# Optimization experiments

Measured on AMD Instinct MI355X. Metric: run time of the kernel, lower is better.

The kernel has to match this reference:

```python
import jax, jax.numpy as jnp
import numpy as np

B, N, E = 32, 128, 8192        # graphs, nodes/graph, edges total
IN, ED, H = 64, 32, 128        # node feat, edge feat, hidden
K1, K2, K3 = 64, 32, 16        # ceil(0.5*N) cascade from TopKPooling(ratio=0.5)
EPS = 1e-5


def setup_inputs():
    key = jax.random.key(0)
    ks = jax.random.split(key, 20)
    def rn(i, shape, s=1.0):
        return jax.random.normal(ks[i], shape, dtype=jnp.float32) * s
    x = rn(0, (B * N, IN))
    edge_attr = rn(1, (E, ED))
    epg = E // B  # edges per graph (intra-graph only)
    src = jax.random.randint(ks[2], (B, epg), 0, N)
    dst = jax.random.randint(ks[3], (B, epg), 0, N)
    off = (jnp.arange(B) * N)[:, None]
    edge_index = jnp.stack([(src + off).reshape(-1), (dst + off).reshape(-1)]).astype(jnp.int32)
    batch = jnp.repeat(jnp.arange(B), N).astype(jnp.int32)
    p = {}
    p['nn1_w'] = rn(4, (ED, IN * H), 0.05); p['nn1_b'] = jnp.zeros((IN * H,), jnp.float32)
    p['root1'] = rn(5, (IN, H), 0.1);       p['bias1'] = jnp.zeros((H,), jnp.float32)
    p['nn2_w'] = rn(6, (ED, H * H), 0.05);  p['nn2_b'] = jnp.zeros((H * H,), jnp.float32)
    p['root2'] = rn(7, (H, H), 0.1);        p['bias2'] = jnp.zeros((H,), jnp.float32)
    p['nn3_w'] = rn(8, (ED, H * H), 0.05);  p['nn3_b'] = jnp.zeros((H * H,), jnp.float32)
    p['root3'] = rn(9, (H, H), 0.1);        p['bias3'] = jnp.zeros((H,), jnp.float32)
    for k in ('1', '2', '3'):
        p['gamma' + k] = jnp.ones((H,), jnp.float32)
        p['beta' + k] = jnp.zeros((H,), jnp.float32)
    p['pw1'] = rn(10, (H,), 0.1); p['pw2'] = rn(11, (H,), 0.1); p['pw3'] = rn(12, (H,), 0.1)
    p['lin1_w'] = rn(13, (H, H // 2), 0.1); p['lin1_b'] = jnp.zeros((H // 2,), jnp.float32)
    p['lin2_w'] = rn(14, (H // 2, 1), 0.1); p['lin2_b'] = jnp.zeros((1,), jnp.float32)
    return dict(x=x, edge_index=edge_index, edge_attr=edge_attr, batch=batch, **p)


def _nnconv(x, src, dst, emask, eattr, nn_w, nn_b, root, bias, cin, cout, n_nodes):
    # per-edge weight matrix from edge MLP: [E, cin, cout]
    w = (eattr @ nn_w + nn_b).reshape(-1, cin, cout)
    msg = jnp.einsum('ei,eio->eo', x[src], w) * emask[:, None]  # per-edge matvec
    agg = jnp.zeros((n_nodes, cout), x.dtype).at[dst].add(msg)  # scatter-add aggr
    return agg + x @ root + bias


def _bn(x, gamma, beta):
    mu = x.mean(0)
    var = x.var(0)
    return gamma * (x - mu) * jax.lax.rsqrt(var + EPS) + beta


def _topk_pool(x, src, dst, emask, pw, nb, npg, k):
    # PyG TopKPooling: score = tanh((x.p)/||p||); keep top ceil(ratio*n) per graph
    score = jnp.tanh((x @ pw) / jnp.linalg.norm(pw))            # [nb*npg]
    _, idx = jax.lax.top_k(score.reshape(nb, npg), k)           # [nb, k]
    perm = (idx + (jnp.arange(nb) * npg)[:, None]).reshape(-1)  # global node ids
    x_new = x[perm] * score[perm][:, None]
    mapping = jnp.full((nb * npg,), -1, jnp.int32).at[perm].set(
        jnp.arange(nb * k, dtype=jnp.int32))
    ns, nd = mapping[src], mapping[dst]
    valid = (ns >= 0) & (nd >= 0) & emask   # filter_adj via mask, static shapes
    return x_new, jnp.where(valid, ns, 0), jnp.where(valid, nd, 0), valid


def _forward(x, edge_attr, nn1_w, nn1_b, root1, bias1, gamma1, beta1, pw1,
             nn2_w, nn2_b, root2, bias2, gamma2, beta2, pw2,
             nn3_w, nn3_b, root3, bias3, gamma3, beta3, pw3,
             lin1_w, lin1_b, lin2_w, lin2_b, edge_index):
    src0, dst0 = edge_index[0], edge_index[1]
    m0 = jnp.ones((E,), bool)
    h = _nnconv(x, src0, dst0, m0, edge_attr, nn1_w, nn1_b, root1, bias1, IN, H, B * N)
    h = jax.nn.relu(_bn(h, gamma1, beta1))
    h, s1, d1, m1 = _topk_pool(h, src0, dst0, m0, pw1, B, N, K1)
    h = _nnconv(h, s1, d1, m1, edge_attr, nn2_w, nn2_b, root2, bias2, H, H, B * K1)
    h = jax.nn.relu(_bn(h, gamma2, beta2))
    h, s2, d2, m2 = _topk_pool(h, s1, d1, m1, pw2, B, K1, K2)
    h = _nnconv(h, s2, d2, m2, edge_attr, nn3_w, nn3_b, root3, bias3, H, H, B * K2)
    h = jax.nn.relu(_bn(h, gamma3, beta3))
    h, _, _, _ = _topk_pool(h, s2, d2, m2, pw3, B, K2, K3)
    g = h.reshape(B, K3, H).mean(axis=1)          # global_mean_pool (equal-size graphs)
    g = jax.nn.relu(g @ lin1_w + lin1_b)          # dropout is identity in eval mode
    return jax.nn.sigmoid(g @ lin2_w + lin2_b)    # [B, 1]


def reference(x, edge_index, edge_attr, batch,
              nn1_w, nn1_b, root1, bias1, nn2_w, nn2_b, root2, bias2,
              nn3_w, nn3_b, root3, bias3, gamma1, beta1, gamma2, beta2,
              gamma3, beta3, pw1, pw2, pw3, lin1_w, lin1_b, lin2_w, lin2_b):
    return _forward(x, edge_attr, nn1_w, nn1_b, root1, bias1, gamma1, beta1, pw1,
                    nn2_w, nn2_b, root2, bias2, gamma2, beta2, pw2,
                    nn3_w, nn3_b, root3, bias3, gamma3, beta3, pw3,
                    lin1_w, lin1_b, lin2_w, lin2_b, edge_index)
```

## Files before the change

kernel.cpp:

```cpp
#include <hip/hip_runtime.h>

#define E_TOT 8192
#define NB    32
#define H     128
#define EPG   256
#define NDT   34
#define YD    33
#define YCOLS (YD * H)

typedef __attribute__((ext_vector_type(8))) short bf16x8;
typedef __attribute__((ext_vector_type(4))) float f32x4;

__device__ __forceinline__ unsigned short bf16_rne(float f) {
    unsigned int u = __float_as_uint(f);
    unsigned int r = (u + 0x7FFFu + ((u >> 16) & 1u)) >> 16;
    return (unsigned short)r;
}
__device__ __forceinline__ float bf16_to_f32(unsigned short h) {
    return __uint_as_float(((unsigned int)h) << 16);
}

__device__ __forceinline__ void gload_lds16(const void* g, void* l) {
    __builtin_amdgcn_global_load_lds(
        (const __attribute__((address_space(1))) unsigned int*)g,
        (__attribute__((address_space(3))) unsigned int*)l, 16, 0, 0);
}

template<int CIN>
__global__ __launch_bounds__(128)
void build_A(const float* __restrict__ x, unsigned short* __restrict__ A)
{
    const int v = blockIdx.x;
    unsigned short* row = A + (size_t)v * (3 * CIN);
    for (int i = threadIdx.x; i < CIN; i += 128) {
        const float val = x[(size_t)v * CIN + i];
        const unsigned short h = bf16_rne(val);
        const unsigned short l = bf16_rne(val - bf16_to_f32(h));
        row[i] = h; row[CIN + i] = h; row[2 * CIN + i] = l;
    }
}

template<int CIN>
__global__ __launch_bounds__(256)
void build_Bt(const float* __restrict__ nnw, const float* __restrict__ nnb,
              const float* __restrict__ root, unsigned short* __restrict__ Bt)
{
    const int d  = blockIdx.x;
    const int i0 = blockIdx.y * 32;
    const float* __restrict__ W =
        (d < 32) ? (nnw + (size_t)d * CIN * 128) : ((d == 32) ? nnb : root);

    __shared__ unsigned short LHI[128][40];
    __shared__ unsigned short LLO[128][40];

    for (int idx = threadIdx.x; idx < 32 * 128; idx += 256) {
        const int ii = idx >> 7, o = idx & 127;
        const float val = W[(size_t)(i0 + ii) * 128 + o];
        const unsigned short h = bf16_rne(val);
        const unsigned short l = bf16_rne(val - bf16_to_f32(h));
        LHI[o][ii] = h; LLO[o][ii] = l;
    }
    __syncthreads();

    const int o    = threadIdx.x & 127;
    const int half = threadIdx.x >> 7;
    unsigned short* dst = Bt + (size_t)(d * 128 + o) * (3 * CIN);
    const uint4* hs = (const uint4*)&LHI[o][0];
    const uint4* ls = (const uint4*)&LLO[o][0];
    if (half == 0) {
        uint4* p = (uint4*)(dst + i0);
        p[0] = hs[0]; p[1] = hs[1]; p[2] = hs[2]; p[3] = hs[3];
        uint4* q = (uint4*)(dst + 2 * CIN + i0);
        q[0] = ls[0]; q[1] = ls[1]; q[2] = ls[2]; q[3] = ls[3];
    } else {
        uint4* p = (uint4*)(dst + CIN + i0);
        p[0] = hs[0]; p[1] = hs[1]; p[2] = hs[2]; p[3] = hs[3];
    }
}

template<int K3>
__global__ __launch_bounds__(256)
void ygemm_mfma(const unsigned short* __restrict__ A,
                const unsigned short* __restrict__ Bt,
                float* __restrict__ Y,
                const float* __restrict__ bias,
                float* __restrict__ h)
{
    __shared__ unsigned short Alds[128 * 32];
    __shared__ unsigned short Blds[128 * 32];

    const int lane = threadIdx.x & 63;
    const int w    = threadIdx.x >> 6;
    const int wm = w >> 1, wn = w & 1;
    const int v0 = blockIdx.x * 128;
    const int n0 = blockIdx.y * 128;

    f32x4 acc[4][4];
    #pragma unroll
    for (int i = 0; i < 4; ++i)
        #pragma unroll
        for (int j = 0; j < 4; ++j)
            acc[i][j] = (f32x4)(0.0f);

    const int arow = lane >> 2;
    const int acol = (lane & 3) * 8;
    const int koff = (lane >> 4) * 8;
    const int mrow = lane & 15;

    for (int k0 = 0; k0 < K3; k0 += 32) {
        __syncthreads();
        #pragma unroll
        for (int t = 0; t < 2; ++t) {
            const int c = w * 2 + t;
            const int r = c * 16 + arow;
            gload_lds16(A  + (size_t)(v0 + r) * K3 + k0 + acol, &Alds[c * 512]);
            gload_lds16(Bt + (size_t)(n0 + r) * K3 + k0 + acol, &Blds[c * 512]);
        }
        __syncthreads();

        bf16x8 a[4], b[4];
        #pragma unroll
        for (int f = 0; f < 4; ++f) {
            a[f] = *(const bf16x8*)&Alds[(wm * 64 + f * 16 + mrow) * 32 + koff];
            b[f] = *(const bf16x8*)&Blds[(wn * 64 + f * 16 + mrow) * 32 + koff];
        }
        #pragma unroll
        for (int fm = 0; fm < 4; ++fm)
            #pragma unroll
            for (int fn = 0; fn < 4; ++fn)
                acc[fm][fn] = __builtin_amdgcn_mfma_f32_16x16x32_bf16(
                    a[fm], b[fn], acc[fm][fn], 0, 0, 0);
    }

    const int crow = (lane >> 4) * 4;
    const int ccol = lane & 15;
    const bool is_root = (blockIdx.y == YD);
    #pragma unroll
    for (int fm = 0; fm < 4; ++fm) {
        const int gr = v0 + wm * 64 + fm * 16 + crow;
        #pragma unroll
        for (int fn = 0; fn < 4; ++fn) {
            const int col = wn * 64 + fn * 16 + ccol;
            if (is_root) {
                const float bv = bias[col];
                #pragma unroll
                for (int r = 0; r < 4; ++r)
                    h[(size_t)(gr + r) * H + col] = acc[fm][fn][r] + bv;
            } else {
                const size_t gc = (size_t)blockIdx.y * H + col;
                #pragma unroll
                for (int r = 0; r < 4; ++r)
                    Y[(size_t)(gr + r) * YCOLS + gc] = acc[fm][fn][r];
            }
        }
    }
}

__global__ __launch_bounds__(256)
void contract_edges(const float* __restrict__ Y,
                    const float* __restrict__ ea,
                    const int*   __restrict__ esrc,
                    const int*   __restrict__ edst,
                    float*       __restrict__ agg)
{
    const int grp = threadIdx.x >> 5;
    const int l5  = threadIdx.x & 31;
    const int e   = blockIdx.x * 8 + grp;
    const int s   = esrc[e];
    if (s < 0) return;

    const float* yb  = Y + (size_t)s * YCOLS + l5 * 4;
    const float* ear = ea + (size_t)e * 32;

    float4 acc = *reinterpret_cast<const float4*>(yb + 32 * H);
    #pragma unroll 8
    for (int dd = 0; dd < 32; ++dd) {
        const float c = ear[dd];
        const float4 y = *reinterpret_cast<const float4*>(yb + dd * H);
        acc.x += c * y.x; acc.y += c * y.y; acc.z += c * y.z; acc.w += c * y.w;
    }
    float* out = agg + (size_t)edst[e] * H + l5 * 4;
    atomicAdd(out + 0, acc.x);
    atomicAdd(out + 1, acc.y);
    atomicAdd(out + 2, acc.z);
    atomicAdd(out + 3, acc.w);
}

__global__ __launch_bounds__(256)
void bn_stats(const float* __restrict__ h, int n,
              float* __restrict__ gsum, float* __restrict__ gsumsq)
{
    const int tid   = threadIdx.x;
    const int col   = tid & 127;
    const int rhalf = tid >> 7;
    float s = 0.f, sq = 0.f;
    for (int r = blockIdx.x * 2 + rhalf; r < n; r += gridDim.x * 2) {
        float v = h[(size_t)r * H + col];
        s += v; sq += v * v;
    }
    __shared__ float sh[256];
    sh[tid] = s;  __syncthreads();
    if (rhalf == 0) s += sh[tid + 128];
    __syncthreads();
    sh[tid] = sq; __syncthreads();
    if (rhalf == 0) {
        sq += sh[tid + 128];
        atomicAdd(&gsum[col], s);
        atomicAdd(&gsumsq[col], sq);
    }
}

__global__ __launch_bounds__(256)
void fused_pool(const float* __restrict__ h,
                const float* __restrict__ gsum, const float* __restrict__ gsumsq,
                float n_f,
                const float* __restrict__ gamma, const float* __restrict__ beta,
                const float* __restrict__ pw,
                int npg, int k,
                const int* __restrict__ esrc_in, const int* __restrict__ edst_in,
                int* __restrict__ esrc_out, int* __restrict__ edst_out,
                unsigned short* __restrict__ Aout)
{
    const int g   = blockIdx.x;
    const int tid = threadIdx.x;
    const int wv  = tid >> 6;
    const int ln  = tid & 63;

    __shared__ float muL[128], rsL[128], gmL[128], btL[128], pwL[128];
    __shared__ float scoreL[128], red[128];
    __shared__ int   mapL[128];
    __shared__ float sinv;

    if (tid < 128) {
        const float mu  = gsum[tid] / n_f;
        const float var = gsumsq[tid] / n_f - mu * mu;
        muL[tid] = mu;
        rsL[tid] = rsqrtf(var + 1e-5f);
        gmL[tid] = gamma[tid];
        btL[tid] = beta[tid];
        const float p = pw[tid];
        pwL[tid] = p;
        red[tid] = p * p;
    }
    __syncthreads();
    for (int off = 64; off > 0; off >>= 1) {
        if (tid < off) red[tid] += red[tid + off];
        __syncthreads();
    }
    if (tid == 0) sinv = rsqrtf(red[0]);
    __syncthreads();

    for (int r = wv; r < npg; r += 4) {
        const float* hr = h + (size_t)(g * npg + r) * H;
        float p = 0.f;
        #pragma unroll
        for (int half = 0; half < 2; ++half) {
            const int c = ln + half * 64;
            const float y = fmaxf(gmL[c] * (hr[c] - muL[c]) * rsL[c] + btL[c], 0.f);
            p += y * pwL[c];
        }
        #pragma unroll
        for (int off = 32; off > 0; off >>= 1)
            p += __shfl_down(p, off, 64);
        if (ln == 0) scoreL[r] = tanhf(p * sinv);
    }
    __syncthreads();

    if (tid < npg) {
        const float si = scoreL[tid];
        int cnt = 0;
        for (int j = 0; j < npg; ++j) {
            const float sj = scoreL[j];
            cnt += (sj > si) || (sj == si && j < tid);
        }
        mapL[tid] = (cnt < k) ? cnt : -1;
    }
    __syncthreads();

    for (int r = wv; r < npg; r += 4) {
        const int nr = mapL[r];
        if (nr < 0) continue;
        const float sc = scoreL[r];
        const float* hr = h + (size_t)(g * npg + r) * H;
        unsigned short* arow = Aout + (size_t)(g * k + nr) * 384;
        #pragma unroll
        for (int half = 0; half < 2; ++half) {
            const int c = ln + half * 64;
            const float y = fmaxf(gmL[c] * (hr[c] - muL[c]) * rsL[c] + btL[c], 0.f) * sc;
            const unsigned short hb = bf16_rne(y);
            const unsigned short lb = bf16_rne(y - bf16_to_f32(hb));
            arow[c] = hb; arow[128 + c] = hb; arow[256 + c] = lb;
        }
    }

    {
        const int e = g * EPG + tid;
        const int s = esrc_in[e];
        int ns = -1, nd = -1;
        if (s >= 0) {
            const int ms = mapL[s - g * npg];
            const int md = mapL[edst_in[e] - g * npg];
            if (ms >= 0 && md >= 0) { ns = g * k + ms; nd = g * k + md; }
        }
        esrc_out[e] = ns; edst_out[e] = nd;
    }
}

__global__ __launch_bounds__(256)
void fused_pool_final(const float* __restrict__ h,
                      const float* __restrict__ gsum, const float* __restrict__ gsumsq,
                      float n_f,
                      const float* __restrict__ gamma, const float* __restrict__ beta,
                      const float* __restrict__ pw,
                      const float* __restrict__ lin1_w, const float* __restrict__ lin1_b,
                      const float* __restrict__ lin2_w, const float* __restrict__ lin2_b,
                      float* __restrict__ out)
{
    const int g   = blockIdx.x;
    const int tid = threadIdx.x;
    const int wv  = tid >> 6;
    const int ln  = tid & 63;
    const int npg = 32, k = 16;

    __shared__ float muL[128], rsL[128], gmL[128], btL[128], pwL[128];
    __shared__ float scoreL[32], red[128], gmean[128], h1c[64];
    __shared__ int   mapL[32];
    __shared__ float sinv;

    if (tid < 128) {
        const float mu  = gsum[tid] / n_f;
        const float var = gsumsq[tid] / n_f - mu * mu;
        muL[tid] = mu;
        rsL[tid] = rsqrtf(var + 1e-5f);
        gmL[tid] = gamma[tid];
        btL[tid] = beta[tid];
        const float p = pw[tid];
        pwL[tid] = p;
        red[tid] = p * p;
    }
    __syncthreads();
    for (int off = 64; off > 0; off >>= 1) {
        if (tid < off) red[tid] += red[tid + off];
        __syncthreads();
    }
    if (tid == 0) sinv = rsqrtf(red[0]);
    __syncthreads();

    for (int r = wv; r < npg; r += 4) {
        const float* hr = h + (size_t)(g * npg + r) * H;
        float p = 0.f;
        #pragma unroll
        for (int half = 0; half < 2; ++half) {
            const int c = ln + half * 64;
            const float y = fmaxf(gmL[c] * (hr[c] - muL[c]) * rsL[c] + btL[c], 0.f);
            p += y * pwL[c];
        }
        #pragma unroll
        for (int off = 32; off > 0; off >>= 1)
            p += __shfl_down(p, off, 64);
        if (ln == 0) scoreL[r] = tanhf(p * sinv);
    }
    __syncthreads();

    if (tid < npg) {
        const float si = scoreL[tid];
        int cnt = 0;
        for (int j = 0; j < npg; ++j) {
            const float sj = scoreL[j];
            cnt += (sj > si) || (sj == si && j < tid);
        }
        mapL[tid] = (cnt < k) ? cnt : -1;
    }
    __syncthreads();

    if (tid < 128) {
        float acc = 0.f;
        for (int r = 0; r < npg; ++r) {
            if (mapL[r] < 0) continue;
            const float hv = h[(size_t)(g * npg + r) * H + tid];
            const float y  = fmaxf(gmL[tid] * (hv - muL[tid]) * rsL[tid] + btL[tid], 0.f);
            acc += y * scoreL[r];
        }
        gmean[tid] = acc * (1.0f / 16.0f);
    }
    __syncthreads();

    if (tid < 64) {
        float acc = lin1_b[tid];
        for (int o = 0; o < 128; ++o) acc += gmean[o] * lin1_w[o * 64 + tid];
        h1c[tid] = fmaxf(acc, 0.f);
    }
    __syncthreads();
    if (tid == 0) {
        float z = lin2_b[0];
        for (int j = 0; j < 64; ++j) z += h1c[j] * lin2_w[j];
        out[g] = 1.0f / (1.0f + expf(-z));
    }
}

extern "C" void kernel_launch(void* const* d_in, const int* in_sizes, int n_in,
                              void* d_out, int out_size, void* d_ws, size_t ws_size,
                              hipStream_t stream)
{
    const float* x        = (const float*)d_in[0];
    const int*   ei       = (const int*)  d_in[1];
    const float* eattr    = (const float*)d_in[2];
    const float* nn1_w    = (const float*)d_in[4];
    const float* nn1_b    = (const float*)d_in[5];
    const float* root1    = (const float*)d_in[6];
    const float* bias1    = (const float*)d_in[7];
    const float* nn2_w    = (const float*)d_in[8];
    const float* nn2_b    = (const float*)d_in[9];
    const float* root2    = (const float*)d_in[10];
    const float* bias2    = (const float*)d_in[11];
    const float* nn3_w    = (const float*)d_in[12];
    const float* nn3_b    = (const float*)d_in[13];
    const float* root3    = (const float*)d_in[14];
    const float* bias3    = (const float*)d_in[15];
    const float* gamma1   = (const float*)d_in[16];
    const float* beta1    = (const float*)d_in[17];
    const float* gamma2   = (const float*)d_in[18];
    const float* beta2    = (const float*)d_in[19];
    const float* gamma3   = (const float*)d_in[20];
    const float* beta3    = (const float*)d_in[21];
    const float* pw1      = (const float*)d_in[22];
    const float* pw2      = (const float*)d_in[23];
    const float* pw3      = (const float*)d_in[24];
    const float* lin1_w   = (const float*)d_in[25];
    const float* lin1_b   = (const float*)d_in[26];
    const float* lin2_w   = (const float*)d_in[27];
    const float* lin2_b   = (const float*)d_in[28];

    const int* ei_src = ei;
    const int* ei_dst = ei + E_TOT;

    char* wp = (char*)d_ws;
    auto alloc = [&](size_t bytes) { char* p = wp; wp += (bytes + 255) & ~(size_t)255; return p; };
    float* h1   = (float*)alloc(4096 * 128 * 4);
    float* h2   = (float*)alloc(2048 * 128 * 4);
    float* h3   = (float*)alloc(1024 * 128 * 4);
    int*   src1 = (int*)alloc(E_TOT * 4);
    int*   dst1 = (int*)alloc(E_TOT * 4);
    int*   src2 = (int*)alloc(E_TOT * 4);
    int*   dst2 = (int*)alloc(E_TOT * 4);
    float* stats = (float*)alloc(6 * 128 * 4);
    unsigned short* A1  = (unsigned short*)alloc((size_t)4096 * 192 * 2);
    unsigned short* A2  = (unsigned short*)alloc((size_t)2048 * 384 * 2);
    unsigned short* A3  = (unsigned short*)alloc((size_t)1024 * 384 * 2);
    unsigned short* Bt1 = (unsigned short*)alloc((size_t)4352 * 192 * 2);
    unsigned short* Bt2 = (unsigned short*)alloc((size_t)4352 * 384 * 2);
    unsigned short* Bt3 = (unsigned short*)alloc((size_t)4352 * 384 * 2);
    float* Ybuf = (float*)alloc((size_t)4096 * YCOLS * 4);

    hipMemsetAsync(stats, 0, 6 * 128 * sizeof(float), stream);

    build_Bt<64> <<<dim3(NDT, 2), 256, 0, stream>>>(nn1_w, nn1_b, root1, Bt1);
    build_Bt<128><<<dim3(NDT, 4), 256, 0, stream>>>(nn2_w, nn2_b, root2, Bt2);
    build_Bt<128><<<dim3(NDT, 4), 256, 0, stream>>>(nn3_w, nn3_b, root3, Bt3);
    build_A<64><<<4096, 128, 0, stream>>>(x, A1);

    ygemm_mfma<192><<<dim3(32, NDT), 256, 0, stream>>>(A1, Bt1, Ybuf, bias1, h1);
    contract_edges<<<E_TOT / 8, 256, 0, stream>>>(Ybuf, eattr, ei_src, ei_dst, h1);
    bn_stats<<<64, 256, 0, stream>>>(h1, 4096, stats, stats + 128);
    fused_pool<<<NB, 256, 0, stream>>>(h1, stats, stats + 128, 4096.0f,
                                       gamma1, beta1, pw1, 128, 64,
                                       ei_src, ei_dst, src1, dst1, A2);

    ygemm_mfma<384><<<dim3(16, NDT), 256, 0, stream>>>(A2, Bt2, Ybuf, bias2, h2);
    contract_edges<<<E_TOT / 8, 256, 0, stream>>>(Ybuf, eattr, src1, dst1, h2);
    bn_stats<<<64, 256, 0, stream>>>(h2, 2048, stats + 256, stats + 384);
    fused_pool<<<NB, 256, 0, stream>>>(h2, stats + 256, stats + 384, 2048.0f,
                                       gamma2, beta2, pw2, 64, 32,
                                       src1, dst1, src2, dst2, A3);

    ygemm_mfma<384><<<dim3(8, NDT), 256, 0, stream>>>(A3, Bt3, Ybuf, bias3, h3);
    contract_edges<<<E_TOT / 8, 256, 0, stream>>>(Ybuf, eattr, src2, dst2, h3);
    bn_stats<<<64, 256, 0, stream>>>(h3, 1024, stats + 512, stats + 640);
    fused_pool_final<<<NB, 256, 0, stream>>>(h3, stats + 512, stats + 640, 1024.0f,
                                             gamma3, beta3, pw3,
                                             lin1_w, lin1_b, lin2_w, lin2_b,
                                             (float*)d_out);
}
```

Before: 318.0 us.

## Store split-bf16 operands once and widen GEMM tile to 128x256

The A and Bt operand buffers now hold only the hi and lo bf16 halves instead of a duplicated hi copy, which shrinks them by a third. The GEMM kernel rebuilds the three split-precision products (hi*hi, hi*lo, lo*hi) by choosing K offsets per iteration. It also widens the output tile to 256 columns per block, each wave covering 128 columns with 32 accumulators. This cuts operand memory traffic and build-kernel writes and improves B reuse, at the cost of higher register pressure and fewer blocks in the grid.

```diff
diff --git a/kernel.cpp b/kernel.cpp
--- a/kernel.cpp
+++ b/kernel.cpp
@@ -4,7 +4,6 @@
 #define NB    32
 #define H     128
 #define EPG   256
-#define NDT   34
 #define YD    33
 #define YCOLS (YD * H)
 
@@ -19,7 +18,6 @@
 __device__ __forceinline__ float bf16_to_f32(unsigned short h) {
     return __uint_as_float(((unsigned int)h) << 16);
 }
-
 __device__ __forceinline__ void gload_lds16(const void* g, void* l) {
     __builtin_amdgcn_global_load_lds(
         (const __attribute__((address_space(1))) unsigned int*)g,
@@ -31,12 +29,12 @@
 void build_A(const float* __restrict__ x, unsigned short* __restrict__ A)
 {
     const int v = blockIdx.x;
-    unsigned short* row = A + (size_t)v * (3 * CIN);
+    unsigned short* row = A + (size_t)v * (2 * CIN);
     for (int i = threadIdx.x; i < CIN; i += 128) {
         const float val = x[(size_t)v * CIN + i];
         const unsigned short h = bf16_rne(val);
         const unsigned short l = bf16_rne(val - bf16_to_f32(h));
-        row[i] = h; row[CIN + i] = h; row[2 * CIN + i] = l;
+        row[i] = h; row[CIN + i] = l;
     }
 }
 
@@ -64,93 +62,112 @@
 
     const int o    = threadIdx.x & 127;
     const int half = threadIdx.x >> 7;
-    unsigned short* dst = Bt + (size_t)(d * 128 + o) * (3 * CIN);
-    const uint4* hs = (const uint4*)&LHI[o][0];
-    const uint4* ls = (const uint4*)&LLO[o][0];
+    unsigned short* dst = Bt + (size_t)(d * 128 + o) * (2 * CIN);
     if (half == 0) {
+        const uint4* hs = (const uint4*)&LHI[o][0];
         uint4* p = (uint4*)(dst + i0);
         p[0] = hs[0]; p[1] = hs[1]; p[2] = hs[2]; p[3] = hs[3];
-        uint4* q = (uint4*)(dst + 2 * CIN + i0);
+    } else {
+        const uint4* ls = (const uint4*)&LLO[o][0];
+        uint4* q = (uint4*)(dst + CIN + i0);
         q[0] = ls[0]; q[1] = ls[1]; q[2] = ls[2]; q[3] = ls[3];
-    } else {
-        uint4* p = (uint4*)(dst + CIN + i0);
-        p[0] = hs[0]; p[1] = hs[1]; p[2] = hs[2]; p[3] = hs[3];
-    }
-}
-
-template<int K3>
+    }
+}
+
+template<int CIN>
 __global__ __launch_bounds__(256)
-void ygemm_mfma(const unsigned short* __restrict__ A,
-                const unsigned short* __restrict__ Bt,
-                float* __restrict__ Y,
-                const float* __restrict__ bias,
-                float* __restrict__ h)
-{
+void ygemm2(const unsigned short* __restrict__ A,
+            const unsigned short* __restrict__ Bt,
+            float* __restrict__ Y,
+            const float* __restrict__ bias,
+            float* __restrict__ h)
+{
+    constexpr int K2 = 2 * CIN;
+    constexpr int CH = CIN / 32;
+    constexpr int NC = 3 * CH;
     __shared__ unsigned short Alds[128 * 32];
-    __shared__ unsigned short Blds[128 * 32];
-
-    const int lane = threadIdx.x & 63;
-    const int w    = threadIdx.x >> 6;
+    __shared__ unsigned short Blds[256 * 32];
+
+    const int tid  = threadIdx.x;
+    const int lane = tid & 63;
+    const int w    = tid >> 6;
     const int wm = w >> 1, wn = w & 1;
     const int v0 = blockIdx.x * 128;
-    const int n0 = blockIdx.y * 128;
-
-    f32x4 acc[4][4];
+    const int n0 = blockIdx.y * 256;
+
+    f32x4 acc[4][8];
     #pragma unroll
     for (int i = 0; i < 4; ++i)
         #pragma unroll
-        for (int j = 0; j < 4; ++j)
+        for (int j = 0; j < 8; ++j)
             acc[i][j] = (f32x4)(0.0f);
 
-    const int arow = lane >> 2;
-    const int acol = (lane & 3) * 8;
+    const int srow = lane >> 2;
+    const int sseg = (lane & 3) * 8;
     const int koff = (lane >> 4) * 8;
     const int mrow = lane & 15;
 
-    for (int k0 = 0; k0 < K3; k0 += 32) {
+    for (int kk = 0; kk < NC; ++kk) {
+        const int r = kk / CH, c = kk % CH;
+        const int a_k = (r < 2) ? c * 32 : CIN + c * 32;
+        const int b_k = (r == 1) ? CIN + c * 32 : c * 32;
+
         __syncthreads();
         #pragma unroll
         for (int t = 0; t < 2; ++t) {
-            const int c = w * 2 + t;
-            const int r = c * 16 + arow;
-            gload_lds16(A  + (size_t)(v0 + r) * K3 + k0 + acol, &Alds[c * 512]);
-            gload_lds16(Bt + (size_t)(n0 + r) * K3 + k0 + acol, &Blds[c * 512]);
+            const int ch = w * 2 + t;
+            gload_lds16(A + (size_t)(v0 + ch * 16 + srow) * K2 + a_k + sseg,
+                        &Alds[ch * 512]);
+        }
+        #pragma unroll
+        for (int t = 0; t < 4; ++t) {
+            const int ch = w * 4 + t;
+            gload_lds16(Bt + (size_t)(n0 + ch * 16 + srow) * K2 + b_k + sseg,
+                        &Blds[ch * 512]);
         }
         __syncthreads();
 
-        bf16x8 a[4], b[4];
-        #pragma unroll
-        for (int f = 0; f < 4; ++f) {
+        bf16x8 a[4], b[8];
+        #pragma unroll
+        for (int f = 0; f < 4; ++f)
             a[f] = *(const bf16x8*)&Alds[(wm * 64 + f * 16 + mrow) * 32 + koff];
-            b[f] = *(const bf16x8*)&Blds[(wn * 64 + f * 16 + mrow) * 32 + koff];
-        }
+        #pragma unroll
+        for (int f = 0; f < 8; ++f)
+            b[f] = *(const bf16x8*)&Blds[(wn * 128 + f * 16 + mrow) * 32 + koff];
         #pragma unroll
         for (int fm = 0; fm < 4; ++fm)
             #pragma unroll
-            for (int fn = 0; fn < 4; ++fn)
+            for (int fn = 0; fn < 8; ++fn)
                 acc[fm][fn] = __builtin_amdgcn_mfma_f32_16x16x32_bf16(
                     a[fm], b[fn], acc[fm][fn], 0, 0, 0);
     }
 
     const int crow = (lane >> 4) * 4;
     const int ccol = lane & 15;
-    const bool is_root = (blockIdx.y == YD);
-    #pragma unroll
-    for (int fm = 0; fm < 4; ++fm) {
-        const int gr = v0 + wm * 64 + fm * 16 + crow;
-        #pragma unroll
-        for (int fn = 0; fn < 4; ++fn) {
-            const int col = wn * 64 + fn * 16 + ccol;
-            if (is_root) {
+    const int dblk = blockIdx.y * 2 + wn;
+    if (dblk == YD) {
+        #pragma unroll
+        for (int fm = 0; fm < 4; ++fm) {
+            const int gr = v0 + wm * 64 + fm * 16 + crow;
+            #pragma unroll
+            for (int fn = 0; fn < 8; ++fn) {
+                const int col = fn * 16 + ccol;
                 const float bv = bias[col];
                 #pragma unroll
-                for (int r = 0; r < 4; ++r)
-                    h[(size_t)(gr + r) * H + col] = acc[fm][fn][r] + bv;
-            } else {
-                const size_t gc = (size_t)blockIdx.y * H + col;
+                for (int rr = 0; rr < 4; ++rr)
+                    h[(size_t)(gr + rr) * H + col] = acc[fm][fn][rr] + bv;
+            }
+        }
+    } else {
+        #pragma unroll
+        for (int fm = 0; fm < 4; ++fm) {
+            const int gr = v0 + wm * 64 + fm * 16 + crow;
+            #pragma unroll
+            for (int fn = 0; fn < 8; ++fn) {
+                const size_t gc = (size_t)dblk * H + fn * 16 + ccol;
                 #pragma unroll
-                for (int r = 0; r < 4; ++r)
-                    Y[(size_t)(gr + r) * YCOLS + gc] = acc[fm][fn][r];
+                for (int rr = 0; rr < 4; ++rr)
+                    Y[(size_t)(gr + rr) * YCOLS + gc] = acc[fm][fn][rr];
             }
         }
     }
@@ -282,14 +299,14 @@
         if (nr < 0) continue;
         const float sc = scoreL[r];
         const float* hr = h + (size_t)(g * npg + r) * H;
-        unsigned short* arow = Aout + (size_t)(g * k + nr) * 384;
+        unsigned short* arow = Aout + (size_t)(g * k + nr) * 256;
         #pragma unroll
         for (int half = 0; half < 2; ++half) {
             const int c = ln + half * 64;
             const float y = fmaxf(gmL[c] * (hr[c] - muL[c]) * rsL[c] + btL[c], 0.f) * sc;
             const unsigned short hb = bf16_rne(y);
             const unsigned short lb = bf16_rne(y - bf16_to_f32(hb));
-            arow[c] = hb; arow[128 + c] = hb; arow[256 + c] = lb;
+            arow[c] = hb; arow[128 + c] = lb;
         }
     }
 
@@ -436,44 +453,44 @@
 
     char* wp = (char*)d_ws;
     auto alloc = [&](size_t bytes) { char* p = wp; wp += (bytes + 255) & ~(size_t)255; return p; };
-    float* h1   = (float*)alloc(4096 * 128 * 4);
-    float* h2   = (float*)alloc(2048 * 128 * 4);
-    float* h3   = (float*)alloc(1024 * 128 * 4);
-    int*   src1 = (int*)alloc(E_TOT * 4);
-    int*   dst1 = (int*)alloc(E_TOT * 4);
-    int*   src2 = (int*)alloc(E_TOT * 4);
-    int*   dst2 = (int*)alloc(E_TOT * 4);
+    float* h1    = (float*)alloc(4096 * 128 * 4);
+    float* h2    = (float*)alloc(2048 * 128 * 4);
+    float* h3    = (float*)alloc(1024 * 128 * 4);
+    int*   src1  = (int*)alloc(E_TOT * 4);
+    int*   dst1  = (int*)alloc(E_TOT * 4);
+    int*   src2  = (int*)alloc(E_TOT * 4);
+    int*   dst2  = (int*)alloc(E_TOT * 4);
     float* stats = (float*)alloc(6 * 128 * 4);
-    unsigned short* A1  = (unsigned short*)alloc((size_t)4096 * 192 * 2);
-    unsigned short* A2  = (unsigned short*)alloc((size_t)2048 * 384 * 2);
-    unsigned short* A3  = (unsigned short*)alloc((size_t)1024 * 384 * 2);
-    unsigned short* Bt1 = (unsigned short*)alloc((size_t)4352 * 192 * 2);
-    unsigned short* Bt2 = (unsigned short*)alloc((size_t)4352 * 384 * 2);
-    unsigned short* Bt3 = (unsigned short*)alloc((size_t)4352 * 384 * 2);
+    unsigned short* A1  = (unsigned short*)alloc((size_t)4096 * 128 * 2);
+    unsigned short* A2  = (unsigned short*)alloc((size_t)2048 * 256 * 2);
+    unsigned short* A3  = (unsigned short*)alloc((size_t)1024 * 256 * 2);
+    unsigned short* Bt1 = (unsigned short*)alloc((size_t)4352 * 128 * 2);
+    unsigned short* Bt2 = (unsigned short*)alloc((size_t)4352 * 256 * 2);
+    unsigned short* Bt3 = (unsigned short*)alloc((size_t)4352 * 256 * 2);
     float* Ybuf = (float*)alloc((size_t)4096 * YCOLS * 4);
 
     hipMemsetAsync(stats, 0, 6 * 128 * sizeof(float), stream);
 
-    build_Bt<64> <<<dim3(NDT, 2), 256, 0, stream>>>(nn1_w, nn1_b, root1, Bt1);
-    build_Bt<128><<<dim3(NDT, 4), 256, 0, stream>>>(nn2_w, nn2_b, root2, Bt2);
-    build_Bt<128><<<dim3(NDT, 4), 256, 0, stream>>>(nn3_w, nn3_b, root3, Bt3);
     build_A<64><<<4096, 128, 0, stream>>>(x, A1);
-
-    ygemm_mfma<192><<<dim3(32, NDT), 256, 0, stream>>>(A1, Bt1, Ybuf, bias1, h1);
+    build_Bt<64> <<<dim3(34, 2), 256, 0, stream>>>(nn1_w, nn1_b, root1, Bt1);
+    build_Bt<128><<<dim3(34, 4), 256, 0, stream>>>(nn2_w, nn2_b, root2, Bt2);
+    build_Bt<128><<<dim3(34, 4), 256, 0, stream>>>(nn3_w, nn3_b, root3, Bt3);
+
+    ygemm2<64><<<dim3(32, 17), 256, 0, stream>>>(A1, Bt1, Ybuf, bias1, h1);
     contract_edges<<<E_TOT / 8, 256, 0, stream>>>(Ybuf, eattr, ei_src, ei_dst, h1);
     bn_stats<<<64, 256, 0, stream>>>(h1, 4096, stats, stats + 128);
     fused_pool<<<NB, 256, 0, stream>>>(h1, stats, stats + 128, 4096.0f,
                                        gamma1, beta1, pw1, 128, 64,
                                        ei_src, ei_dst, src1, dst1, A2);
 
-    ygemm_mfma<384><<<dim3(16, NDT), 256, 0, stream>>>(A2, Bt2, Ybuf, bias2, h2);
+    ygemm2<128><<<dim3(16, 17), 256, 0, stream>>>(A2, Bt2, Ybuf, bias2, h2);
     contract_edges<<<E_TOT / 8, 256, 0, stream>>>(Ybuf, eattr, src1, dst1, h2);
     bn_stats<<<64, 256, 0, stream>>>(h2, 2048, stats + 256, stats + 384);
     fused_pool<<<NB, 256, 0, stream>>>(h2, stats + 256, stats + 384, 2048.0f,
                                        gamma2, beta2, pw2, 64, 32,
                                        src1, dst1, src2, dst2, A3);
 
-    ygemm_mfma<384><<<dim3(8, NDT), 256, 0, stream>>>(A3, Bt3, Ybuf, bias3, h3);
+    ygemm2<128><<<dim3(8, 17), 256, 0, stream>>>(A3, Bt3, Ybuf, bias3, h3);
     contract_edges<<<E_TOT / 8, 256, 0, stream>>>(Ybuf, eattr, src2, dst2, h3);
     bn_stats<<<64, 256, 0, stream>>>(h3, 1024, stats + 512, stats + 640);
     fused_pool_final<<<NB, 256, 0, stream>>>(h3, stats + 512, stats + 640, 1024.0f,
```

Result: slower. 342.8 us (+7.8%).
